# Kernel optimization log

Hardware: AMD Instinct MI355X
Metric: run time of the kernel (lower is better)

Reference implementation:

```python
import jax, jax.numpy as jnp
import numpy as np

B, S, D = 16, 577, 768   # batch, seq_len=(384//16)**2+1, hidden
H = 12                   # num heads
Dh = D // H              # head dim = 64
EPS = 1e-5


def setup_inputs() -> dict:
    key = jax.random.key(0)
    ks = jax.random.split(key, 12)
    sd = 0.02
    return {
        "x":    jax.random.normal(ks[0], (B, S, D), jnp.float32),
        "Wq":   jax.random.normal(ks[1], (D, 2 * D), jnp.float32) * sd,
        "bq":   jnp.zeros((2 * D,), jnp.float32),
        "Wk":   jax.random.normal(ks[2], (D, 2 * D), jnp.float32) * sd,
        "bk":   jnp.zeros((2 * D,), jnp.float32),
        "Wv":   jax.random.normal(ks[3], (D, D), jnp.float32) * sd,
        "bv":   jnp.zeros((D,), jnp.float32),
        "Wo":   jax.random.normal(ks[4], (D, D), jnp.float32) * sd,
        "bo":   jnp.zeros((D,), jnp.float32),
        "lam":  jnp.float32(0.5),
        "gn_w": jnp.ones((D,), jnp.float32),
        "gn_b": jnp.zeros((D,), jnp.float32),
    }


def _split_heads(t):
    # [B,S,D] -> [B,H,S,Dh]
    return t.reshape(B, S, H, Dh).transpose(0, 2, 1, 3)


def reference(x, Wq, bq, Wk, bk, Wv, bv, Wo, bo, lam, gn_w, gn_b):
    qc = x @ Wq + bq                      # [B,S,2D]
    kc = x @ Wk + bk
    v = _split_heads(x @ Wv + bv)         # [B,H,S,Dh]
    q1, q2 = _split_heads(qc[..., :D]), _split_heads(qc[..., D:])
    k1, k2 = _split_heads(kc[..., :D]), _split_heads(kc[..., D:])

    scale = 1.0 / np.sqrt(Dh).astype(np.float32)
    p1 = jax.nn.softmax(jnp.einsum('bhqd,bhkd->bhqk', q1, k1) * scale, axis=-1)
    p2 = jax.nn.softmax(jnp.einsum('bhqd,bhkd->bhqk', q2, k2) * scale, axis=-1)
    diff = p1 - lam * p2                  # [B,H,S,S] (dropout is identity at eval)
    ctx = jnp.einsum('bhqk,bhkd->bhqd', diff, v)   # [B,H,S,Dh]

    # GroupNorm path, faithfully reproducing the torch reshapes:
    # [B,H,S,Dh] -> permute -> [B,H,Dh,S] -> view [B, H*Dh, S]
    c = ctx.transpose(0, 1, 3, 2).reshape(B, H * Dh, S)
    g = c.reshape(B, H, Dh * S)
    mu = g.mean(axis=-1, keepdims=True)
    var = g.var(axis=-1, keepdims=True)
    g = (g - mu) * jax.lax.rsqrt(var + EPS)
    c = g.reshape(B, H * Dh, S) * gn_w[None, :, None] + gn_b[None, :, None]
    # torch then does permute(0,2,1).contiguous(); transpose(1,2).contiguous().view(B,S,D)
    # which nets out to reinterpreting the [B, H*Dh, S] buffer as [B, S, D]:
    context = c.reshape(B, S, D)

    out = context @ Wo + bo               # [B,S,D]
    return out
```

## Files before the change

kernel.cpp:

```cpp
#include <hip/hip_runtime.h>
#include <hip/hip_bf16.h>
#include <stdint.h>

typedef unsigned short u16;
typedef __attribute__((ext_vector_type(8))) short bf16x8;
typedef __attribute__((ext_vector_type(4))) float f32x4;

#define S_LEN 577
#define DMODEL 768
#define NHEAD 12
#define DH 64
#define BATCH 16
#define M_ROWS (BATCH * S_LEN)
#define M_PAD 9344
#define VT_STRIDE 640

__device__ __forceinline__ u16 f2bu(float f) {
  uint32_t u = __float_as_uint(f);
  u += 0x7FFFu + ((u >> 16) & 1u);
  return (u16)(u >> 16);
}
__device__ __forceinline__ float bu2f(u16 b) {
  return __uint_as_float(((uint32_t)b) << 16);
}
__device__ __forceinline__ void gl2lds16(const u16* g, u16* l) {
  __builtin_amdgcn_global_load_lds(
      (const __attribute__((address_space(1))) unsigned int*)g,
      (__attribute__((address_space(3))) unsigned int*)l, 16, 0, 0);
}

__global__ __launch_bounds__(256) void prep_x(const float* __restrict__ x,
                                              u16* __restrict__ xb) {
  int e = (blockIdx.x * 256 + threadIdx.x) * 8;
  u16 o[8];
  if (e < M_ROWS * DMODEL) {
    float4 f0 = *(const float4*)(x + e);
    float4 f1 = *(const float4*)(x + e + 4);
    o[0] = f2bu(f0.x); o[1] = f2bu(f0.y); o[2] = f2bu(f0.z); o[3] = f2bu(f0.w);
    o[4] = f2bu(f1.x); o[5] = f2bu(f1.y); o[6] = f2bu(f1.z); o[7] = f2bu(f1.w);
  } else {
#pragma unroll
    for (int i = 0; i < 8; ++i) o[i] = 0;
  }
  *(uint4*)(xb + e) = *(const uint4*)o;
}

__global__ __launch_bounds__(256) void prep_w(
    const float* __restrict__ Wq, const float* __restrict__ Wk,
    const float* __restrict__ Wv, const float* __restrict__ Wo,
    u16* __restrict__ wtqkv, u16* __restrict__ wot) {
  __shared__ u16 tile[32][33];
  int blk = blockIdx.x;
  const float* W; int N; u16* dst; int rowbase;
  if (blk < 1152)      { W = Wq; N = 1536; dst = wtqkv; rowbase = 0; }
  else if (blk < 2304) { W = Wk; N = 1536; dst = wtqkv; rowbase = 1536; blk -= 1152; }
  else if (blk < 2880) { W = Wv; N = 768;  dst = wtqkv; rowbase = 3072; blk -= 2304; }
  else                 { W = Wo; N = 768;  dst = wot;   rowbase = 0;    blk -= 2880; }
  const int ntiles = N >> 5;
  const int tk = blk / ntiles, tn = blk - tk * ntiles;
  const int c = threadIdx.x & 31, r0 = threadIdx.x >> 5;
#pragma unroll
  for (int i = 0; i < 4; ++i) {
    int r = i * 8 + r0;
    tile[r][c] = f2bu(W[(size_t)(tk * 32 + r) * N + tn * 32 + c]);
  }
  __syncthreads();
#pragma unroll
  for (int i = 0; i < 4; ++i) {
    int r = i * 8 + r0;
    dst[(size_t)(rowbase + tn * 32 + r) * 768 + tk * 32 + c] = tile[c][r];
  }
}

__global__ __launch_bounds__(256, 2) void gemm_bf16(
    const u16* __restrict__ A, const u16* __restrict__ Bt, int N, int mode,
    float* __restrict__ outF, const float* __restrict__ biasO,
    u16* __restrict__ q1p, u16* __restrict__ q2p,
    u16* __restrict__ k1p, u16* __restrict__ k2p, u16* __restrict__ vtp,
    const float* __restrict__ bq, const float* __restrict__ bk,
    const float* __restrict__ bvp) {
  __shared__ __align__(16) u16 smem[16384];
  const int t = threadIdx.x;
  const int lane = t & 63, wave = t >> 6;
  const int quad = lane >> 4, l16 = lane & 15;
  const int wm = wave & 1, wn = wave >> 1;

  const int NTg = gridDim.y;
  const int nwg = 73 * NTg;
  const int lin = blockIdx.y * 73 + blockIdx.x;
  const int xcd8 = lin & 7;
  const int idx8 = lin >> 3;
  const int qq = nwg >> 3, rr = nwg & 7;
  const int slot = (xcd8 < rr) ? xcd8 * (qq + 1) + idx8
                               : rr * (qq + 1) + (xcd8 - rr) * qq + idx8;
  const int C = (NTg >= 10) ? 5 : NTg;
  const int bpc = 73 * C;
  const int chunk = slot / bpc;
  const int rem = slot - chunk * bpc;
  const int mt = rem / C;
  const int nt = chunk * C + (rem - mt * C);
  const int m0 = mt * 128;
  const int n0 = nt * 128;

  f32x4 zero = {0.f, 0.f, 0.f, 0.f};
  f32x4 acc[4][4];
  for (int i = 0; i < 4; ++i) for (int j = 0; j < 4; ++j) acc[i][j] = zero;

  const int srow = wave * 32 + (lane >> 2);
  const int scol = (lane & 3) * 8;
  const u16* gA = A + (size_t)(m0 + srow) * 768 + scol;
  const u16* gB = Bt + (size_t)(n0 + srow) * 768 + scol;
  const int wofs = wave * 1024;

  {
    u16* sA = smem + wofs;
    u16* sB = smem + 4096 + wofs;
    gl2lds16(gA, sA);
    gl2lds16(gA + 16 * 768, sA + 512);
    gl2lds16(gB, sB);
    gl2lds16(gB + 16 * 768, sB + 512);
  }
  __syncthreads();

  int cur = 0;
  for (int k0 = 0; k0 < 768; k0 += 32) {
    if (k0 < 736) {
      u16* sA = smem + (cur ^ 1) * 8192 + wofs;
      u16* sB = smem + (cur ^ 1) * 8192 + 4096 + wofs;
      gl2lds16(gA + k0 + 32, sA);
      gl2lds16(gA + k0 + 32 + 16 * 768, sA + 512);
      gl2lds16(gB + k0 + 32, sB);
      gl2lds16(gB + k0 + 32 + 16 * 768, sB + 512);
    }
    const u16* cA = smem + cur * 8192;
    const u16* cB = smem + cur * 8192 + 4096;
    bf16x8 af[4], bfr[4];
#pragma unroll
    for (int i = 0; i < 4; ++i)
      af[i] = *(const bf16x8*)(cA + (wm * 64 + i * 16 + l16) * 32 + quad * 8);
#pragma unroll
    for (int j = 0; j < 4; ++j)
      bfr[j] = *(const bf16x8*)(cB + (wn * 64 + j * 16 + l16) * 32 + quad * 8);
#pragma unroll
    for (int i = 0; i < 4; ++i)
#pragma unroll
      for (int j = 0; j < 4; ++j)
        acc[i][j] = __builtin_amdgcn_mfma_f32_16x16x32_bf16(af[i], bfr[j], acc[i][j], 0, 0, 0);
    __syncthreads();
    cur ^= 1;
  }

  if (mode == 0) {
#pragma unroll
    for (int i = 0; i < 4; ++i) {
#pragma unroll
      for (int j = 0; j < 4; ++j) {
        int n = n0 + wn * 64 + j * 16 + l16;
#pragma unroll
        for (int r = 0; r < 4; ++r) {
          int m = m0 + wm * 64 + i * 16 + quad * 4 + r;
          if (m >= M_ROWS) continue;
          outF[(size_t)m * N + n] = acc[i][j][r] + biasO[n];
        }
      }
    }
    return;
  }

  u16* tile = smem;
  const bool isv = (n0 >= 3072);
  u16* dstqk = nullptr; const float* biasp = nullptr; int ch0 = 0;
  if (!isv) {
    if (n0 < 768)       { dstqk = q1p; biasp = bq + n0;          ch0 = n0; }
    else if (n0 < 1536) { dstqk = q2p; biasp = bq + n0;          ch0 = n0 - 768; }
    else if (n0 < 2304) { dstqk = k1p; biasp = bk + (n0 - 1536); ch0 = n0 - 1536; }
    else                { dstqk = k2p; biasp = bk + (n0 - 1536); ch0 = n0 - 2304; }
  }
  const int ch0v = n0 - 3072;

#pragma unroll
  for (int hf = 0; hf < 2; ++hf) {
    __syncthreads();
    if (wn == hf) {
      if (!isv) {
        float bfv[4];
#pragma unroll
        for (int j = 0; j < 4; ++j) bfv[j] = biasp[hf * 64 + j * 16 + l16];
#pragma unroll
        for (int i = 0; i < 4; ++i)
#pragma unroll
          for (int j = 0; j < 4; ++j) {
            int col = j * 16 + l16;
#pragma unroll
            for (int r = 0; r < 4; ++r) {
              int m = wm * 64 + i * 16 + quad * 4 + r;
              int addr = m * 64 + (col & 15) + ((((col >> 4) ^ (m & 3)) & 3) << 4);
              tile[addr] = f2bu(acc[i][j][r] + bfv[j]);
            }
          }
      } else {
        float bfv[4];
#pragma unroll
        for (int j = 0; j < 4; ++j) bfv[j] = bvp[ch0v + hf * 64 + j * 16 + l16];
#pragma unroll
        for (int i = 0; i < 4; ++i)
#pragma unroll
          for (int j = 0; j < 4; ++j) {
            int d = j * 16 + l16;
#pragma unroll
            for (int r = 0; r < 4; ++r) {
              int m = wm * 64 + i * 16 + quad * 4 + r;
              int addr = d * 128 + (m & 15) + ((((m >> 4) ^ (d & 7)) & 7) << 4);
              tile[addr] = f2bu(acc[i][j][r] + bfv[j]);
            }
          }
      }
    }
    __syncthreads();

    if (!isv) {
      const int line = t >> 3;
      const int col0 = (t & 7) * 8;
      const int head = (ch0 >> 6) + hf;
#pragma unroll
      for (int p = 0; p < 4; ++p) {
        int m = p * 32 + line;
        int mg = m0 + m;
        if (mg < M_ROWS) {
          int addr = m * 64 + (col0 & 15) + ((((col0 >> 4) ^ (m & 3)) & 3) << 4);
          uint4 v4 = *(const uint4*)(tile + addr);
          int b = mg / 577;
          int s = mg - b * 577;
          *(uint4*)(dstqk + (((size_t)(b * 12 + head) * 577 + s) * 64 + col0)) = v4;
        }
      }
    } else {
      const int line = t >> 4;
      const int col0 = (t & 15) * 8;
      const int hh = (ch0v >> 6) + hf;
#pragma unroll
      for (int p = 0; p < 4; ++p) {
        int d = p * 16 + line;
        int addr = d * 128 + (col0 & 15) + ((((col0 >> 4) ^ (d & 7)) & 7) << 4);
        uint4 v4 = *(const uint4*)(tile + addr);
        int sg0 = m0 + col0;
        int b0 = sg0 / 577, b7 = (sg0 + 7) / 577;
        if (sg0 + 7 < M_ROWS && b0 == b7) {
          *(uint4*)(vtp + (((size_t)(b0 * 12 + hh) * 64 + d) * VT_STRIDE + (sg0 - b0 * 577))) = v4;
        } else {
          const u16* ev = (const u16*)&v4;
          for (int e = 0; e < 8; ++e) {
            int sg = sg0 + e;
            if (sg >= M_ROWS) break;
            int bb = sg / 577;
            vtp[((size_t)(bb * 12 + hh) * 64 + d) * VT_STRIDE + (sg - bb * 577)] = ev[e];
          }
        }
      }
    }
  }
}

__global__ __launch_bounds__(256, 4) void attn(
    const u16* __restrict__ q1, const u16* __restrict__ q2,
    const u16* __restrict__ k1, const u16* __restrict__ k2,
    const u16* __restrict__ vt, u16* __restrict__ ctx_t,
    const float* __restrict__ lam_p) {
  __shared__ u16 sk1[2][2048];
  __shared__ u16 sk2[2][2048];
  __shared__ u16 sv[2][2048];
  __shared__ u16 pls[4][2][16 * 40];

  const int tid = threadIdx.x;
  const int wave = tid >> 6;
  const int lane = tid & 63;
  const int quad = lane >> 4, l16 = lane & 15;

  const int bid = blockIdx.x;
  const int xcd = bid & 7;
  const int slot = bid >> 3;
  const int bhl = slot / 10;
  const int qgroup = slot - bhl * 10;
  const int bh = xcd * 24 + bhl;
  const int q0 = (qgroup * 4 + wave) * 16;

  const float lam = lam_p[0];
  const float CEXP = 0.125f * 1.44269504f;
  const size_t qkbase = (size_t)bh * S_LEN * DH;
  const size_t vbase = (size_t)bh * 64 * VT_STRIDE;

  const int krow = tid >> 3;
  const int kelem = ((((tid & 7) << 4) ^ ((krow & 7) << 4)) >> 1);
  const u16* k1s = k1 + qkbase + (size_t)krow * 64 + kelem;
  const u16* k2s = k2 + qkbase + (size_t)krow * 64 + kelem;
  const int vrow = tid >> 2;
  const int vel = ((((tid & 3) << 4) ^ ((vrow & 3) << 4)) >> 1);
  const u16* vs = vt + vbase + (size_t)vrow * VT_STRIDE + vel;
  const int w512 = wave * 512;

  int qr = q0 + l16; if (qr > 576) qr = 576;
  bf16x8 q1f[2], q2f[2];
#pragma unroll
  for (int c = 0; c < 2; ++c) {
    q1f[c] = *(const bf16x8*)(q1 + qkbase + (size_t)qr * 64 + c * 32 + quad * 8);
    q2f[c] = *(const bf16x8*)(q2 + qkbase + (size_t)qr * 64 + c * 32 + quad * 8);
  }

  f32x4 zero = {0.f, 0.f, 0.f, 0.f};
  f32x4 O1[4], O2[4];
  float l1[4], l2[4];
#pragma unroll
  for (int i = 0; i < 4; ++i) { O1[i] = zero; O2[i] = zero; l1[i] = 0.f; l2[i] = 0.f; }

  u16* p1w = &pls[wave][0][0];
  u16* p2w = &pls[wave][1][0];

  const int xk = (l16 & 7) << 4;
  const int xv = (l16 & 3) << 4;

  gl2lds16(k1s, &sk1[0][0] + w512);
  gl2lds16(k2s, &sk2[0][0] + w512);
  gl2lds16(vs, &sv[0][0] + w512);
  __syncthreads();

  int cur = 0;
  for (int kb = 0; kb < 18; ++kb) {
    if (kb < 17) {
      gl2lds16(k1s + (kb + 1) * 2048, &sk1[cur ^ 1][0] + w512);
      gl2lds16(k2s + (kb + 1) * 2048, &sk2[cur ^ 1][0] + w512);
      gl2lds16(vs + (kb + 1) * 32, &sv[cur ^ 1][0] + w512);
    } else {
      gl2lds16(k1 + qkbase + 576 * 64 + kelem, &sk1[cur ^ 1][0] + w512);
      gl2lds16(k2 + qkbase + 576 * 64 + kelem, &sk2[cur ^ 1][0] + w512);
      gl2lds16(vs + 576, &sv[cur ^ 1][0] + w512);
    }

    const char* bk1 = (const char*)&sk1[cur][0];
    const char* bk2 = (const char*)&sk2[cur][0];
    const char* bv = (const char*)&sv[cur][0];
    bf16x8 k1f[2][2], k2f[2][2], vf[4];
#pragma unroll
    for (int tt = 0; tt < 2; ++tt) {
      int rb = (tt * 16 + l16) * 128;
      k1f[tt][0] = *(const bf16x8*)(bk1 + rb + ((quad * 16) ^ xk));
      k1f[tt][1] = *(const bf16x8*)(bk1 + rb + ((64 + quad * 16) ^ xk));
      k2f[tt][0] = *(const bf16x8*)(bk2 + rb + ((quad * 16) ^ xk));
      k2f[tt][1] = *(const bf16x8*)(bk2 + rb + ((64 + quad * 16) ^ xk));
    }
#pragma unroll
    for (int tt = 0; tt < 4; ++tt)
      vf[tt] = *(const bf16x8*)(bv + (tt * 16 + l16) * 64 + ((quad * 16) ^ xv));

    f32x4 s1[2], s2[2];
    __builtin_amdgcn_s_setprio(1);
#pragma unroll
    for (int tt = 0; tt < 2; ++tt) {
      s1[tt] = __builtin_amdgcn_mfma_f32_16x16x32_bf16(q1f[0], k1f[tt][0], zero, 0, 0, 0);
      s1[tt] = __builtin_amdgcn_mfma_f32_16x16x32_bf16(q1f[1], k1f[tt][1], s1[tt], 0, 0, 0);
      s2[tt] = __builtin_amdgcn_mfma_f32_16x16x32_bf16(q2f[0], k2f[tt][0], zero, 0, 0, 0);
      s2[tt] = __builtin_amdgcn_mfma_f32_16x16x32_bf16(q2f[1], k2f[tt][1], s2[tt], 0, 0, 0);
    }
    __builtin_amdgcn_s_setprio(0);

#pragma unroll
    for (int i = 0; i < 4; ++i) {
      float p10 = exp2f(s1[0][i] * CEXP);
      float p11 = exp2f(s1[1][i] * CEXP);
      float p20 = exp2f(s2[0][i] * CEXP);
      float p21 = exp2f(s2[1][i] * CEXP);
      l1[i] += p10 + p11;
      l2[i] += p20 + p21;
      p1w[(quad * 4 + i) * 40 + l16]      = (u16)(__float_as_uint(p10) >> 16);
      p1w[(quad * 4 + i) * 40 + l16 + 16] = (u16)(__float_as_uint(p11) >> 16);
      p2w[(quad * 4 + i) * 40 + l16]      = (u16)(__float_as_uint(p20) >> 16);
      p2w[(quad * 4 + i) * 40 + l16 + 16] = (u16)(__float_as_uint(p21) >> 16);
    }
    bf16x8 p1a = *(const bf16x8*)(p1w + l16 * 40 + quad * 8);
    bf16x8 p2a = *(const bf16x8*)(p2w + l16 * 40 + quad * 8);
    __builtin_amdgcn_s_setprio(1);
#pragma unroll
    for (int tt = 0; tt < 4; ++tt) {
      O1[tt] = __builtin_amdgcn_mfma_f32_16x16x32_bf16(p1a, vf[tt], O1[tt], 0, 0, 0);
      O2[tt] = __builtin_amdgcn_mfma_f32_16x16x32_bf16(p2a, vf[tt], O2[tt], 0, 0, 0);
    }
    __builtin_amdgcn_s_setprio(0);
    __syncthreads();
    cur ^= 1;
  }

  {
    const char* bk1 = (const char*)&sk1[cur][0];
    const char* bk2 = (const char*)&sk2[cur][0];
    const char* bv = (const char*)&sv[cur][0];
    int rb = l16 * 128;
    bf16x8 ka0 = *(const bf16x8*)(bk1 + rb + ((quad * 16) ^ xk));
    bf16x8 ka1 = *(const bf16x8*)(bk1 + rb + ((64 + quad * 16) ^ xk));
    bf16x8 kb0 = *(const bf16x8*)(bk2 + rb + ((quad * 16) ^ xk));
    bf16x8 kb1 = *(const bf16x8*)(bk2 + rb + ((64 + quad * 16) ^ xk));
    f32x4 s1t = __builtin_amdgcn_mfma_f32_16x16x32_bf16(q1f[0], ka0, zero, 0, 0, 0);
    s1t = __builtin_amdgcn_mfma_f32_16x16x32_bf16(q1f[1], ka1, s1t, 0, 0, 0);
    f32x4 s2t = __builtin_amdgcn_mfma_f32_16x16x32_bf16(q2f[0], kb0, zero, 0, 0, 0);
    s2t = __builtin_amdgcn_mfma_f32_16x16x32_bf16(q2f[1], kb1, s2t, 0, 0, 0);
    bf16x8 vf[4];
#pragma unroll
    for (int tt = 0; tt < 4; ++tt)
      vf[tt] = *(const bf16x8*)(bv + (tt * 16 + l16) * 64 + ((quad * 16) ^ xv));
    bool ok = (l16 == 0);
#pragma unroll
    for (int i = 0; i < 4; ++i) {
      float p10 = ok ? exp2f(s1t[i] * CEXP) : 0.f;
      float p20 = ok ? exp2f(s2t[i] * CEXP) : 0.f;
      l1[i] += p10; l2[i] += p20;
      p1w[(quad * 4 + i) * 40 + l16]      = (u16)(__float_as_uint(p10) >> 16);
      p1w[(quad * 4 + i) * 40 + l16 + 16] = 0;
      p2w[(quad * 4 + i) * 40 + l16]      = (u16)(__float_as_uint(p20) >> 16);
      p2w[(quad * 4 + i) * 40 + l16 + 16] = 0;
    }
    bf16x8 p1a = *(const bf16x8*)(p1w + l16 * 40 + quad * 8);
    bf16x8 p2a = *(const bf16x8*)(p2w + l16 * 40 + quad * 8);
#pragma unroll
    for (int tt = 0; tt < 4; ++tt) {
      O1[tt] = __builtin_amdgcn_mfma_f32_16x16x32_bf16(p1a, vf[tt], O1[tt], 0, 0, 0);
      O2[tt] = __builtin_amdgcn_mfma_f32_16x16x32_bf16(p2a, vf[tt], O2[tt], 0, 0, 0);
    }
  }

#pragma unroll
  for (int d = 1; d < 16; d <<= 1)
#pragma unroll
    for (int i = 0; i < 4; ++i) {
      l1[i] += __shfl_xor(l1[i], d);
      l2[i] += __shfl_xor(l2[i], d);
    }
  float inv1[4], inv2[4];
#pragma unroll
  for (int i = 0; i < 4; ++i) { inv1[i] = 1.f / l1[i]; inv2[i] = 1.f / l2[i]; }
#pragma unroll
  for (int tt = 0; tt < 4; ++tt) {
    size_t cb = ((size_t)bh * 64 + tt * 16 + l16) * S_LEN;
#pragma unroll
    for (int i = 0; i < 4; ++i) {
      int s = q0 + quad * 4 + i;
      if (s < S_LEN)
        ctx_t[cb + s] = f2bu(O1[tt][i] * inv1[i] - lam * O2[tt][i] * inv2[i]);
    }
  }
}

__global__ __launch_bounds__(256) void gnorm(
    const u16* __restrict__ ctx_t, u16* __restrict__ context,
    const float* __restrict__ gw, const float* __restrict__ gb) {
  const int bh = blockIdx.x;
  const int h = bh % 12;
  const int NEL = 64 * S_LEN;
  const int NV = NEL / 8;
  const u16* src = ctx_t + (size_t)bh * NEL;
  float sum = 0.f, sq = 0.f;
  for (int v = threadIdx.x; v < NV; v += 256) {
    uint4 raw = *(const uint4*)(src + v * 8);
    uint32_t w[4] = {raw.x, raw.y, raw.z, raw.w};
#pragma unroll
    for (int j = 0; j < 4; ++j) {
      float f0 = bu2f((u16)(w[j] & 0xffff));
      float f1 = bu2f((u16)(w[j] >> 16));
      sum += f0 + f1; sq += f0 * f0 + f1 * f1;
    }
  }
#pragma unroll
  for (int d = 1; d < 64; d <<= 1) {
    sum += __shfl_xor(sum, d);
    sq += __shfl_xor(sq, d);
  }
  __shared__ float rs[4], rq[4];
  __shared__ float wv[64], bv2[64];
  int wave = threadIdx.x >> 6;
  if ((threadIdx.x & 63) == 0) { rs[wave] = sum; rq[wave] = sq; }
  __syncthreads();
  float ts = rs[0] + rs[1] + rs[2] + rs[3];
  float tq = rq[0] + rq[1] + rq[2] + rq[3];
  const float Ninv = 1.0f / (float)NEL;
  float mu = ts * Ninv;
  float var = tq * Ninv - mu * mu;
  float rstd = rsqrtf(var + 1e-5f);
  if (threadIdx.x < 64) {
    float w = gw[h * 64 + threadIdx.x] * rstd;
    wv[threadIdx.x] = w;
    bv2[threadIdx.x] = gb[h * 64 + threadIdx.x] - mu * w;
  }
  __syncthreads();
  u16* dst = context + (size_t)bh * NEL;
  for (int v = threadIdx.x; v < NV; v += 256) {
    uint4 raw = *(const uint4*)(src + v * 8);
    uint32_t w[4] = {raw.x, raw.y, raw.z, raw.w};
    int base = v * 8;
    int d0 = base / 577;
    int r0 = base - d0 * 577;
    u16 o[8];
#pragma unroll
    for (int j = 0; j < 4; ++j) {
#pragma unroll
      for (int e = 0; e < 2; ++e) {
        int ii = j * 2 + e;
        int dd = (r0 + ii >= 577) ? d0 + 1 : d0;
        float f = bu2f((u16)(e == 0 ? (w[j] & 0xffff) : (w[j] >> 16)));
        o[ii] = f2bu(f * wv[dd] + bv2[dd]);
      }
    }
    *(uint4*)(dst + base) = *(const uint4*)o;
  }
}

extern "C" void kernel_launch(void* const* d_in, const int* in_sizes, int n_in,
                              void* d_out, int out_size, void* d_ws, size_t ws_size,
                              hipStream_t stream) {
  const float* x   = (const float*)d_in[0];
  const float* Wq  = (const float*)d_in[1];
  const float* bq  = (const float*)d_in[2];
  const float* Wk  = (const float*)d_in[3];
  const float* bk  = (const float*)d_in[4];
  const float* Wv  = (const float*)d_in[5];
  const float* bv  = (const float*)d_in[6];
  const float* Wo  = (const float*)d_in[7];
  const float* bo  = (const float*)d_in[8];
  const float* lam = (const float*)d_in[9];
  const float* gw  = (const float*)d_in[10];
  const float* gb  = (const float*)d_in[11];
  float* out = (float*)d_out;

  char* p = (char*)d_ws;
  auto alloc = [&](size_t bytes) {
    char* r = p;
    p += (bytes + 255) & ~(size_t)255;
    return r;
  };
  u16* xb     = (u16*)alloc((size_t)M_PAD * 768 * 2);
  u16* wtqkv  = (u16*)alloc((size_t)3840 * 768 * 2);
  u16* wot    = (u16*)alloc((size_t)768 * 768 * 2);
  u16* q1b    = (u16*)alloc((size_t)192 * 577 * 64 * 2);
  u16* q2b    = (u16*)alloc((size_t)192 * 577 * 64 * 2);
  u16* k1b    = (u16*)alloc((size_t)192 * 577 * 64 * 2);
  u16* k2b    = (u16*)alloc((size_t)192 * 577 * 64 * 2);
  u16* vtb    = (u16*)alloc((size_t)192 * 64 * VT_STRIDE * 2);
  u16* ctxt   = (u16*)alloc((size_t)192 * 64 * S_LEN * 2);
  u16* ctxbuf = xb;

  prep_x<<<(M_PAD * 768 / 8 + 255) / 256, 256, 0, stream>>>(x, xb);
  prep_w<<<3456, 256, 0, stream>>>(Wq, Wk, Wv, Wo, wtqkv, wot);

  gemm_bf16<<<dim3(73, 30), 256, 0, stream>>>(xb, wtqkv, 3840, 1,
      nullptr, nullptr, q1b, q2b, k1b, k2b, vtb, bq, bk, bv);

  attn<<<dim3(1920), 256, 0, stream>>>(q1b, q2b, k1b, k2b, vtb, ctxt, lam);

  gnorm<<<192, 256, 0, stream>>>(ctxt, ctxbuf, gw, gb);

  gemm_bf16<<<dim3(73, 6), 256, 0, stream>>>(ctxbuf, wot, 768, 0,
      out, bo, nullptr, nullptr, nullptr, nullptr, nullptr, nullptr, nullptr, nullptr);
}
```

Measured before the change: 306.0 us.

## Fuse GroupNorm statistics into attention epilogue and fold softmax scale into Q

The attention kernel now accumulates per-(batch,head) sum and sum-of-squares of its output in fp32 and adds them to a stats buffer with atomics. The GroupNorm kernel then reads those stats instead of making a separate reduction pass over the context tensor. The softmax scale times log2(e) is folded into Q in the QKV GEMM epilogue, which removes a multiply per score. Waves whose query tile lies entirely past the sequence end also skip compute. This trades one read pass of the context tensor for global atomics and a zeroing step in prep_x, and the stats now come from fp32 values rather than the bf16-rounded ones.

```diff
diff --git a/kernel.cpp b/kernel.cpp
--- a/kernel.cpp
+++ b/kernel.cpp
@@ -14,6 +14,7 @@
 #define M_ROWS (BATCH * S_LEN)
 #define M_PAD 9344
 #define VT_STRIDE 640
+#define CEXPF 0.18033688f
 
 __device__ __forceinline__ u16 f2bu(float f) {
   uint32_t u = __float_as_uint(f);
@@ -30,7 +31,9 @@
 }
 
 __global__ __launch_bounds__(256) void prep_x(const float* __restrict__ x,
-                                              u16* __restrict__ xb) {
+                                              u16* __restrict__ xb,
+                                              float* __restrict__ stats) {
+  if (blockIdx.x == 0 && threadIdx.x < 384) stats[threadIdx.x] = 0.f;
   int e = (blockIdx.x * 256 + threadIdx.x) * 8;
   u16 o[8];
   if (e < M_ROWS * DMODEL) {
@@ -176,6 +179,7 @@
     else if (n0 < 2304) { dstqk = k1p; biasp = bk + (n0 - 1536); ch0 = n0 - 1536; }
     else                { dstqk = k2p; biasp = bk + (n0 - 1536); ch0 = n0 - 2304; }
   }
+  const float qscl = (n0 < 1536) ? CEXPF : 1.0f;
   const int ch0v = n0 - 3072;
 
 #pragma unroll
@@ -195,7 +199,7 @@
             for (int r = 0; r < 4; ++r) {
               int m = wm * 64 + i * 16 + quad * 4 + r;
               int addr = m * 64 + (col & 15) + ((((col >> 4) ^ (m & 3)) & 3) << 4);
-              tile[addr] = f2bu(acc[i][j][r] + bfv[j]);
+              tile[addr] = f2bu((acc[i][j][r] + bfv[j]) * qscl);
             }
           }
       } else {
@@ -265,7 +269,7 @@
     const u16* __restrict__ q1, const u16* __restrict__ q2,
     const u16* __restrict__ k1, const u16* __restrict__ k2,
     const u16* __restrict__ vt, u16* __restrict__ ctx_t,
-    const float* __restrict__ lam_p) {
+    const float* __restrict__ lam_p, float* __restrict__ stats) {
   __shared__ u16 sk1[2][2048];
   __shared__ u16 sk2[2][2048];
   __shared__ u16 sv[2][2048];
@@ -283,9 +287,9 @@
   const int qgroup = slot - bhl * 10;
   const int bh = xcd * 24 + bhl;
   const int q0 = (qgroup * 4 + wave) * 16;
+  const bool active = (q0 < S_LEN);
 
   const float lam = lam_p[0];
-  const float CEXP = 0.125f * 1.44269504f;
   const size_t qkbase = (size_t)bh * S_LEN * DH;
   const size_t vbase = (size_t)bh * 64 * VT_STRIDE;
 
@@ -335,153 +339,152 @@
       gl2lds16(vs + 576, &sv[cur ^ 1][0] + w512);
     }
 
-    const char* bk1 = (const char*)&sk1[cur][0];
-    const char* bk2 = (const char*)&sk2[cur][0];
-    const char* bv = (const char*)&sv[cur][0];
-    bf16x8 k1f[2][2], k2f[2][2], vf[4];
-#pragma unroll
-    for (int tt = 0; tt < 2; ++tt) {
-      int rb = (tt * 16 + l16) * 128;
-      k1f[tt][0] = *(const bf16x8*)(bk1 + rb + ((quad * 16) ^ xk));
-      k1f[tt][1] = *(const bf16x8*)(bk1 + rb + ((64 + quad * 16) ^ xk));
-      k2f[tt][0] = *(const bf16x8*)(bk2 + rb + ((quad * 16) ^ xk));
-      k2f[tt][1] = *(const bf16x8*)(bk2 + rb + ((64 + quad * 16) ^ xk));
-    }
-#pragma unroll
-    for (int tt = 0; tt < 4; ++tt)
-      vf[tt] = *(const bf16x8*)(bv + (tt * 16 + l16) * 64 + ((quad * 16) ^ xv));
-
-    f32x4 s1[2], s2[2];
-    __builtin_amdgcn_s_setprio(1);
-#pragma unroll
-    for (int tt = 0; tt < 2; ++tt) {
-      s1[tt] = __builtin_amdgcn_mfma_f32_16x16x32_bf16(q1f[0], k1f[tt][0], zero, 0, 0, 0);
-      s1[tt] = __builtin_amdgcn_mfma_f32_16x16x32_bf16(q1f[1], k1f[tt][1], s1[tt], 0, 0, 0);
-      s2[tt] = __builtin_amdgcn_mfma_f32_16x16x32_bf16(q2f[0], k2f[tt][0], zero, 0, 0, 0);
-      s2[tt] = __builtin_amdgcn_mfma_f32_16x16x32_bf16(q2f[1], k2f[tt][1], s2[tt], 0, 0, 0);
-    }
-    __builtin_amdgcn_s_setprio(0);
-
-#pragma unroll
-    for (int i = 0; i < 4; ++i) {
-      float p10 = exp2f(s1[0][i] * CEXP);
-      float p11 = exp2f(s1[1][i] * CEXP);
-      float p20 = exp2f(s2[0][i] * CEXP);
-      float p21 = exp2f(s2[1][i] * CEXP);
-      l1[i] += p10 + p11;
-      l2[i] += p20 + p21;
-      p1w[(quad * 4 + i) * 40 + l16]      = (u16)(__float_as_uint(p10) >> 16);
-      p1w[(quad * 4 + i) * 40 + l16 + 16] = (u16)(__float_as_uint(p11) >> 16);
-      p2w[(quad * 4 + i) * 40 + l16]      = (u16)(__float_as_uint(p20) >> 16);
-      p2w[(quad * 4 + i) * 40 + l16 + 16] = (u16)(__float_as_uint(p21) >> 16);
-    }
-    bf16x8 p1a = *(const bf16x8*)(p1w + l16 * 40 + quad * 8);
-    bf16x8 p2a = *(const bf16x8*)(p2w + l16 * 40 + quad * 8);
-    __builtin_amdgcn_s_setprio(1);
-#pragma unroll
-    for (int tt = 0; tt < 4; ++tt) {
-      O1[tt] = __builtin_amdgcn_mfma_f32_16x16x32_bf16(p1a, vf[tt], O1[tt], 0, 0, 0);
-      O2[tt] = __builtin_amdgcn_mfma_f32_16x16x32_bf16(p2a, vf[tt], O2[tt], 0, 0, 0);
-    }
-    __builtin_amdgcn_s_setprio(0);
+    if (active) {
+      const char* bk1 = (const char*)&sk1[cur][0];
+      const char* bk2 = (const char*)&sk2[cur][0];
+      const char* bv = (const char*)&sv[cur][0];
+      bf16x8 k1f[2][2], k2f[2][2], vf[4];
+#pragma unroll
+      for (int tt = 0; tt < 2; ++tt) {
+        int rb = (tt * 16 + l16) * 128;
+        k1f[tt][0] = *(const bf16x8*)(bk1 + rb + ((quad * 16) ^ xk));
+        k1f[tt][1] = *(const bf16x8*)(bk1 + rb + ((64 + quad * 16) ^ xk));
+        k2f[tt][0] = *(const bf16x8*)(bk2 + rb + ((quad * 16) ^ xk));
+        k2f[tt][1] = *(const bf16x8*)(bk2 + rb + ((64 + quad * 16) ^ xk));
+      }
+#pragma unroll
+      for (int tt = 0; tt < 4; ++tt)
+        vf[tt] = *(const bf16x8*)(bv + (tt * 16 + l16) * 64 + ((quad * 16) ^ xv));
+
+      f32x4 s1[2], s2[2];
+      __builtin_amdgcn_s_setprio(1);
+#pragma unroll
+      for (int tt = 0; tt < 2; ++tt) {
+        s1[tt] = __builtin_amdgcn_mfma_f32_16x16x32_bf16(q1f[0], k1f[tt][0], zero, 0, 0, 0);
+        s1[tt] = __builtin_amdgcn_mfma_f32_16x16x32_bf16(q1f[1], k1f[tt][1], s1[tt], 0, 0, 0);
+        s2[tt] = __builtin_amdgcn_mfma_f32_16x16x32_bf16(q2f[0], k2f[tt][0], zero, 0, 0, 0);
+        s2[tt] = __builtin_amdgcn_mfma_f32_16x16x32_bf16(q2f[1], k2f[tt][1], s2[tt], 0, 0, 0);
+      }
+      __builtin_amdgcn_s_setprio(0);
+
+#pragma unroll
+      for (int i = 0; i < 4; ++i) {
+        float p10 = exp2f(s1[0][i]);
+        float p11 = exp2f(s1[1][i]);
+        float p20 = exp2f(s2[0][i]);
+        float p21 = exp2f(s2[1][i]);
+        l1[i] += p10 + p11;
+        l2[i] += p20 + p21;
+        p1w[(quad * 4 + i) * 40 + l16]      = (u16)(__float_as_uint(p10) >> 16);
+        p1w[(quad * 4 + i) * 40 + l16 + 16] = (u16)(__float_as_uint(p11) >> 16);
+        p2w[(quad * 4 + i) * 40 + l16]      = (u16)(__float_as_uint(p20) >> 16);
+        p2w[(quad * 4 + i) * 40 + l16 + 16] = (u16)(__float_as_uint(p21) >> 16);
+      }
+      bf16x8 p1a = *(const bf16x8*)(p1w + l16 * 40 + quad * 8);
+      bf16x8 p2a = *(const bf16x8*)(p2w + l16 * 40 + quad * 8);
+      __builtin_amdgcn_s_setprio(1);
+#pragma unroll
+      for (int tt = 0; tt < 4; ++tt) {
+        O1[tt] = __builtin_amdgcn_mfma_f32_16x16x32_bf16(p1a, vf[tt], O1[tt], 0, 0, 0);
+        O2[tt] = __builtin_amdgcn_mfma_f32_16x16x32_bf16(p2a, vf[tt], O2[tt], 0, 0, 0);
+      }
+      __builtin_amdgcn_s_setprio(0);
+    }
     __syncthreads();
     cur ^= 1;
   }
 
-  {
-    const char* bk1 = (const char*)&sk1[cur][0];
-    const char* bk2 = (const char*)&sk2[cur][0];
-    const char* bv = (const char*)&sv[cur][0];
-    int rb = l16 * 128;
-    bf16x8 ka0 = *(const bf16x8*)(bk1 + rb + ((quad * 16) ^ xk));
-    bf16x8 ka1 = *(const bf16x8*)(bk1 + rb + ((64 + quad * 16) ^ xk));
-    bf16x8 kb0 = *(const bf16x8*)(bk2 + rb + ((quad * 16) ^ xk));
-    bf16x8 kb1 = *(const bf16x8*)(bk2 + rb + ((64 + quad * 16) ^ xk));
-    f32x4 s1t = __builtin_amdgcn_mfma_f32_16x16x32_bf16(q1f[0], ka0, zero, 0, 0, 0);
-    s1t = __builtin_amdgcn_mfma_f32_16x16x32_bf16(q1f[1], ka1, s1t, 0, 0, 0);
-    f32x4 s2t = __builtin_amdgcn_mfma_f32_16x16x32_bf16(q2f[0], kb0, zero, 0, 0, 0);
-    s2t = __builtin_amdgcn_mfma_f32_16x16x32_bf16(q2f[1], kb1, s2t, 0, 0, 0);
-    bf16x8 vf[4];
-#pragma unroll
-    for (int tt = 0; tt < 4; ++tt)
-      vf[tt] = *(const bf16x8*)(bv + (tt * 16 + l16) * 64 + ((quad * 16) ^ xv));
-    bool ok = (l16 == 0);
-#pragma unroll
-    for (int i = 0; i < 4; ++i) {
-      float p10 = ok ? exp2f(s1t[i] * CEXP) : 0.f;
-      float p20 = ok ? exp2f(s2t[i] * CEXP) : 0.f;
-      l1[i] += p10; l2[i] += p20;
-      p1w[(quad * 4 + i) * 40 + l16]      = (u16)(__float_as_uint(p10) >> 16);
-      p1w[(quad * 4 + i) * 40 + l16 + 16] = 0;
-      p2w[(quad * 4 + i) * 40 + l16]      = (u16)(__float_as_uint(p20) >> 16);
-      p2w[(quad * 4 + i) * 40 + l16 + 16] = 0;
-    }
-    bf16x8 p1a = *(const bf16x8*)(p1w + l16 * 40 + quad * 8);
-    bf16x8 p2a = *(const bf16x8*)(p2w + l16 * 40 + quad * 8);
+  if (active) {
+    {
+      const char* bk1 = (const char*)&sk1[cur][0];
+      const char* bk2 = (const char*)&sk2[cur][0];
+      const char* bv = (const char*)&sv[cur][0];
+      int rb = l16 * 128;
+      bf16x8 ka0 = *(const bf16x8*)(bk1 + rb + ((quad * 16) ^ xk));
+      bf16x8 ka1 = *(const bf16x8*)(bk1 + rb + ((64 + quad * 16) ^ xk));
+      bf16x8 kb0 = *(const bf16x8*)(bk2 + rb + ((quad * 16) ^ xk));
+      bf16x8 kb1 = *(const bf16x8*)(bk2 + rb + ((64 + quad * 16) ^ xk));
+      f32x4 s1t = __builtin_amdgcn_mfma_f32_16x16x32_bf16(q1f[0], ka0, zero, 0, 0, 0);
+      s1t = __builtin_amdgcn_mfma_f32_16x16x32_bf16(q1f[1], ka1, s1t, 0, 0, 0);
+      f32x4 s2t = __builtin_amdgcn_mfma_f32_16x16x32_bf16(q2f[0], kb0, zero, 0, 0, 0);
+      s2t = __builtin_amdgcn_mfma_f32_16x16x32_bf16(q2f[1], kb1, s2t, 0, 0, 0);
+      bf16x8 vf[4];
+#pragma unroll
+      for (int tt = 0; tt < 4; ++tt)
+        vf[tt] = *(const bf16x8*)(bv + (tt * 16 + l16) * 64 + ((quad * 16) ^ xv));
+      bool ok = (l16 == 0);
+#pragma unroll
+      for (int i = 0; i < 4; ++i) {
+        float p10 = ok ? exp2f(s1t[i]) : 0.f;
+        float p20 = ok ? exp2f(s2t[i]) : 0.f;
+        l1[i] += p10; l2[i] += p20;
+        p1w[(quad * 4 + i) * 40 + l16]      = (u16)(__float_as_uint(p10) >> 16);
+        p1w[(quad * 4 + i) * 40 + l16 + 16] = 0;
+        p2w[(quad * 4 + i) * 40 + l16]      = (u16)(__float_as_uint(p20) >> 16);
+        p2w[(quad * 4 + i) * 40 + l16 + 16] = 0;
+      }
+      bf16x8 p1a = *(const bf16x8*)(p1w + l16 * 40 + quad * 8);
+      bf16x8 p2a = *(const bf16x8*)(p2w + l16 * 40 + quad * 8);
+#pragma unroll
+      for (int tt = 0; tt < 4; ++tt) {
+        O1[tt] = __builtin_amdgcn_mfma_f32_16x16x32_bf16(p1a, vf[tt], O1[tt], 0, 0, 0);
+        O2[tt] = __builtin_amdgcn_mfma_f32_16x16x32_bf16(p2a, vf[tt], O2[tt], 0, 0, 0);
+      }
+    }
+
+#pragma unroll
+    for (int d = 1; d < 16; d <<= 1)
+#pragma unroll
+      for (int i = 0; i < 4; ++i) {
+        l1[i] += __shfl_xor(l1[i], d);
+        l2[i] += __shfl_xor(l2[i], d);
+      }
+    float inv1[4], inv2[4];
+#pragma unroll
+    for (int i = 0; i < 4; ++i) { inv1[i] = 1.f / l1[i]; inv2[i] = 1.f / l2[i]; }
+
+    float ssum = 0.f, ssq = 0.f;
 #pragma unroll
     for (int tt = 0; tt < 4; ++tt) {
-      O1[tt] = __builtin_amdgcn_mfma_f32_16x16x32_bf16(p1a, vf[tt], O1[tt], 0, 0, 0);
-      O2[tt] = __builtin_amdgcn_mfma_f32_16x16x32_bf16(p2a, vf[tt], O2[tt], 0, 0, 0);
-    }
-  }
-
-#pragma unroll
-  for (int d = 1; d < 16; d <<= 1)
-#pragma unroll
-    for (int i = 0; i < 4; ++i) {
-      l1[i] += __shfl_xor(l1[i], d);
-      l2[i] += __shfl_xor(l2[i], d);
-    }
-  float inv1[4], inv2[4];
-#pragma unroll
-  for (int i = 0; i < 4; ++i) { inv1[i] = 1.f / l1[i]; inv2[i] = 1.f / l2[i]; }
-#pragma unroll
-  for (int tt = 0; tt < 4; ++tt) {
-    size_t cb = ((size_t)bh * 64 + tt * 16 + l16) * S_LEN;
-#pragma unroll
-    for (int i = 0; i < 4; ++i) {
-      int s = q0 + quad * 4 + i;
-      if (s < S_LEN)
-        ctx_t[cb + s] = f2bu(O1[tt][i] * inv1[i] - lam * O2[tt][i] * inv2[i]);
+      size_t cb = ((size_t)bh * 64 + tt * 16 + l16) * S_LEN;
+#pragma unroll
+      for (int i = 0; i < 4; ++i) {
+        int s = q0 + quad * 4 + i;
+        if (s < S_LEN) {
+          float val = O1[tt][i] * inv1[i] - lam * O2[tt][i] * inv2[i];
+          ctx_t[cb + s] = f2bu(val);
+          ssum += val; ssq += val * val;
+        }
+      }
+    }
+#pragma unroll
+    for (int d = 1; d < 64; d <<= 1) {
+      ssum += __shfl_xor(ssum, d);
+      ssq += __shfl_xor(ssq, d);
+    }
+    if (lane == 0) {
+      atomicAdd(&stats[bh * 2], ssum);
+      atomicAdd(&stats[bh * 2 + 1], ssq);
     }
   }
 }
 
 __global__ __launch_bounds__(256) void gnorm(
     const u16* __restrict__ ctx_t, u16* __restrict__ context,
-    const float* __restrict__ gw, const float* __restrict__ gb) {
+    const float* __restrict__ gw, const float* __restrict__ gb,
+    const float* __restrict__ stats) {
   const int bh = blockIdx.x;
   const int h = bh % 12;
   const int NEL = 64 * S_LEN;
   const int NV = NEL / 8;
   const u16* src = ctx_t + (size_t)bh * NEL;
-  float sum = 0.f, sq = 0.f;
-  for (int v = threadIdx.x; v < NV; v += 256) {
-    uint4 raw = *(const uint4*)(src + v * 8);
-    uint32_t w[4] = {raw.x, raw.y, raw.z, raw.w};
-#pragma unroll
-    for (int j = 0; j < 4; ++j) {
-      float f0 = bu2f((u16)(w[j] & 0xffff));
-      float f1 = bu2f((u16)(w[j] >> 16));
-      sum += f0 + f1; sq += f0 * f0 + f1 * f1;
-    }
-  }
-#pragma unroll
-  for (int d = 1; d < 64; d <<= 1) {
-    sum += __shfl_xor(sum, d);
-    sq += __shfl_xor(sq, d);
-  }
-  __shared__ float rs[4], rq[4];
+  const float ts = stats[bh * 2];
+  const float tq = stats[bh * 2 + 1];
+  const float Ninv = 1.0f / (float)NEL;
+  const float mu = ts * Ninv;
+  const float var = tq * Ninv - mu * mu;
+  const float rstd = rsqrtf(var + 1e-5f);
   __shared__ float wv[64], bv2[64];
-  int wave = threadIdx.x >> 6;
-  if ((threadIdx.x & 63) == 0) { rs[wave] = sum; rq[wave] = sq; }
-  __syncthreads();
-  float ts = rs[0] + rs[1] + rs[2] + rs[3];
-  float tq = rq[0] + rq[1] + rq[2] + rq[3];
-  const float Ninv = 1.0f / (float)NEL;
-  float mu = ts * Ninv;
-  float var = tq * Ninv - mu * mu;
-  float rstd = rsqrtf(var + 1e-5f);
   if (threadIdx.x < 64) {
     float w = gw[h * 64 + threadIdx.x] * rstd;
     wv[threadIdx.x] = w;
@@ -542,17 +545,18 @@
   u16* k2b    = (u16*)alloc((size_t)192 * 577 * 64 * 2);
   u16* vtb    = (u16*)alloc((size_t)192 * 64 * VT_STRIDE * 2);
   u16* ctxt   = (u16*)alloc((size_t)192 * 64 * S_LEN * 2);
+  float* stats = (float*)alloc((size_t)192 * 2 * 4);
   u16* ctxbuf = xb;
 
-  prep_x<<<(M_PAD * 768 / 8 + 255) / 256, 256, 0, stream>>>(x, xb);
+  prep_x<<<(M_PAD * 768 / 8 + 255) / 256, 256, 0, stream>>>(x, xb, stats);
   prep_w<<<3456, 256, 0, stream>>>(Wq, Wk, Wv, Wo, wtqkv, wot);
 
   gemm_bf16<<<dim3(73, 30), 256, 0, stream>>>(xb, wtqkv, 3840, 1,
       nullptr, nullptr, q1b, q2b, k1b, k2b, vtb, bq, bk, bv);
 
-  attn<<<dim3(1920), 256, 0, stream>>>(q1b, q2b, k1b, k2b, vtb, ctxt, lam);
-
-  gnorm<<<192, 256, 0, stream>>>(ctxt, ctxbuf, gw, gb);
+  attn<<<dim3(1920), 256, 0, stream>>>(q1b, q2b, k1b, k2b, vtb, ctxt, lam, stats);
+
+  gnorm<<<192, 256, 0, stream>>>(ctxt, ctxbuf, gw, gb, stats);
 
   gemm_bf16<<<dim3(73, 6), 256, 0, stream>>>(ctxbuf, wot, 768, 0,
       out, bo, nullptr, nullptr, nullptr, nullptr, nullptr, nullptr, nullptr, nullptr);
```

New measurement: 295.3 us. 3.5% less time.
